# Optimization experiments

Hardware: AMD Instinct MI355X
Metric: run time of the kernel (lower is better)

Reference implementation:

```python
import jax, jax.numpy as jnp
import numpy as np

N_BINS = 64
INPUT_DIM = 8
R = 1.2
BOUND = 10.0
BETA = 1e-06
N = 2097152


def _mesh_and_elmt():
    m = N_BINS / 2
    idx = jnp.arange(N_BINS + 1, dtype=jnp.float32) - m
    x1L = BOUND * (R - 1.0) / (R ** m - 1.0)
    xr = (1.0 - R ** jnp.abs(idx)) / (1.0 - R)
    xr = jnp.where(idx >= 0, x1L * xr, -x1L * xr)
    xr = (xr + BOUND) / (2.0 * BOUND)
    mesh = jnp.concatenate([jnp.zeros((1,), jnp.float32), xr[1:-1], jnp.ones((1,), jnp.float32)])  # [n_bins+1]
    elmt = mesh[1:] - mesh[:-1]  # [n_bins]
    return mesh, elmt


def _pdf_normalize(p, elmt):
    # pdf: [n_bins+1, d]; F_ref: [n_bins, d] cumulative bin integrals
    p0 = jnp.full((1, INPUT_DIM), BETA, jnp.float32)
    ep = jnp.exp(p)
    px = ep * ((elmt[:-1] + elmt[1:]) / 2.0)[:, None]
    scale = (1.0 - (elmt[0] + elmt[-1]) * BETA / 2.0) / jnp.sum(px, 0, keepdims=True)
    px = scale * ep
    pdf = jnp.concatenate([p0, px, p0], 0)
    cell = (pdf[:-1] + pdf[1:]) / 2.0 * elmt[:, None]  # [n_bins, d]
    F_ref = jnp.concatenate([jnp.zeros((1, INPUT_DIM), jnp.float32),
                             jnp.cumsum(cell, 0)[:N_BINS - 1]], 0)
    return pdf, F_ref


def setup_inputs() -> dict:
    key = jax.random.key(0)
    k1, k2 = jax.random.split(key)
    x = jax.random.normal(k1, (N, INPUT_DIM), dtype=jnp.float32)
    logdet = jnp.zeros((N, 1), dtype=jnp.float32)
    p = jax.random.normal(k2, (N_BINS - 1, INPUT_DIM), dtype=jnp.float32)
    return {"x": x, "logdet": logdet, "p": p}


def reference(x, logdet, p):
    mesh, elmt = _mesh_and_elmt()
    pdf, F_ref = _pdf_normalize(p, elmt)

    xs = (x + BOUND) / (2.0 * BOUND)  # [N, d] in [0,1] for covered points
    k = jnp.searchsorted(mesh, xs, side='right') - 1  # [N, d]
    cover = (k >= 0) & (k <= N_BINS - 1)
    k = jnp.clip(k, 0, N_BINS - 1)
    col = jnp.arange(INPUT_DIM)[None, :]

    v1 = pdf[k, col]            # [N, d]
    v2 = pdf[k + 1, col]
    xm = xs - mesh[k]
    h = elmt[k]
    F_pre = F_ref[k, col]

    y = jnp.where(cover, F_pre + xm * xm / 2.0 * (v2 - v1) / h + xm * v1, xs)
    dld = jnp.where(cover, xm * (v2 - v1) / h + v1, 1.0)
    logdet = logdet + jnp.sum(jnp.log(dld), -1, keepdims=True)

    y = y * 2.0 * BOUND - BOUND
    y = jnp.where(y > BOUND, BETA * (y - BOUND) + BOUND, y)
    logdet = logdet + jnp.sum(jnp.log(jnp.where(y > BOUND, BETA, 1.0)), -1, keepdims=True)
    y = jnp.where(y < -BOUND, BETA * (y + BOUND) - BOUND, y)
    logdet = logdet + jnp.sum(jnp.log(jnp.where(y < -BOUND, BETA, 1.0)), -1, keepdims=True)
    return y, logdet
```

## Files before the change

### kernel.cpp

```cpp
#include <hip/hip_runtime.h>
#include <hip/hip_bf16.h>
#include <math.h>

#define NDIM   8
#define NBINS  64
#define LOG_BETA   (-13.815510557964274f)
#define LN2F       0.69314718055994531f
#define ALPHA      34.0821892f
#define INV_LOG2R  3.80178401692393f

__global__ __launch_bounds__(256, 8) void cdfq_fused(const float* __restrict__ x,
                                                     const float* __restrict__ logdet_in,
                                                     const float* __restrict__ p,
                                                     float* __restrict__ y_out,
                                                     float* __restrict__ ld_out,
                                                     int n)
{
    __shared__ float  mesh[65];
    __shared__ float  elmt[64];
    __shared__ float  sc[NDIM];
    __shared__ float  pdfs[NDIM][65];
    __shared__ float4 stbl[NDIM * NBINS];

    const int t  = threadIdx.x;
    const int T  = gridDim.x * blockDim.x;
    const int i0 = blockIdx.x * blockDim.x + t;
    const int iters = n / T;
    const float4* xv = (const float4*)x;

    float4 Ac, Bc; float Lc;
    if (iters > 0) {
        Ac = xv[2 * (size_t)i0];
        Bc = xv[2 * (size_t)i0 + 1];
        Lc = logdet_in[i0];
    }
    __builtin_amdgcn_sched_barrier(0);

    if (t < 65) {
        float fidx = (float)t - 32.0f;
        float a = fabsf(fidx);
        float x1L = 2.0f / (powf(1.2f, 32.0f) - 1.0f);
        float xr = x1L * (powf(1.2f, a) - 1.0f) / 0.2f;
        xr = (fidx >= 0.0f) ? xr : -xr;
        xr = (xr + 10.0f) / 20.0f;
        if (t == 0)  xr = 0.0f;
        if (t == 64) xr = 1.0f;
        mesh[t] = xr;
    }
    for (int idx = t; idx < 63 * NDIM; idx += 256) {
        int d = idx & 7, k = idx >> 3;
        pdfs[d][k + 1] = expf(p[k * NDIM + d]);
    }
    if (t < NDIM) { pdfs[t][0] = 1e-6f; pdfs[t][64] = 1e-6f; }
    __syncthreads();
    if (t < 64) elmt[t] = mesh[t + 1] - mesh[t];
    __syncthreads();

    if (t < 64) {
        for (int d = 0; d < NDIM; ++d) {
            float w = 0.0f;
            if (t < 63) w = pdfs[d][t + 1] * 0.5f * (elmt[t] + elmt[t + 1]);
            for (int off = 32; off > 0; off >>= 1) w += __shfl_down(w, off);
            if (t == 0) sc[d] = (1.0f - (elmt[0] + elmt[63]) * 5e-7f) / w;
        }
    }
    __syncthreads();
    for (int idx = t; idx < 63 * NDIM; idx += 256) {
        int d = idx & 7, k = idx >> 3;
        pdfs[d][k + 1] *= sc[d];
    }
    __syncthreads();
    if (t < 64) {
        for (int d = 0; d < NDIM; ++d) {
            float c0 = 0.5f * (pdfs[d][t] + pdfs[d][t + 1]) * elmt[t];
            float v = c0;
            for (int off = 1; off < 64; off <<= 1) {
                float w = __shfl_up(v, off);
                if (t >= off) v += w;
            }
            float Fpre = v - c0;
            float v1 = pdfs[d][t];
            float v2 = pdfs[d][t + 1];
            stbl[d * 64 + t] = make_float4(v1, (v2 - v1) / elmt[t], Fpre, mesh[t]);
        }
    }
    __syncthreads();

    auto body = [&](float4 A, float4 B, float Lin, int i) {
        float ld = Lin;
        float xd[8] = {A.x, A.y, A.z, A.w, B.x, B.y, B.z, B.w};
        float yd[8], dd[8];

#pragma unroll
        for (int d = 0; d < 8; ++d) {
            float xo = xd[d];
            float xs = fmaf(xo, 0.05f, 0.5f);
            float u  = fabsf(xo);
            float g  = __log2f(fmaf(ALPHA, u, 1.0f)) * INV_LOG2R;
            int jp = (int)fminf(g, 31.0f);
            int jn = (int)ceilf(fminf(g, 32.0f));
            int k  = (xo >= 0.0f) ? (32 + jp) : (32 - jn);

            float4 tb = stbl[(d << 6) + k];
            float xm  = xs - tb.w;
            bool cov  = (xs >= 0.0f) && (xs < 1.0f);

            float yc = tb.z + xm * fmaf(0.5f * xm, tb.y, tb.x);
            float dl = fmaf(xm, tb.y, tb.x);
            float yy = cov ? yc : xs;
            dd[d]    = cov ? dl : 1.0f;

            yy = fmaf(yy, 20.0f, -10.0f);
            if (yy > 10.0f)  { yy = fmaf(1e-6f, yy - 10.0f, 10.0f);  ld += LOG_BETA; }
            if (yy < -10.0f) { yy = fmaf(1e-6f, yy + 10.0f, -10.0f); ld += LOG_BETA; }
            yd[d] = yy;
        }

        float l01 = __log2f(dd[0] * dd[1]);
        float l23 = __log2f(dd[2] * dd[3]);
        float l45 = __log2f(dd[4] * dd[5]);
        float l67 = __log2f(dd[6] * dd[7]);
        ld = fmaf((l01 + l23) + (l45 + l67), LN2F, ld);

        float4* yo = (float4*)y_out + 2 * (size_t)i;
        yo[0] = make_float4(yd[0], yd[1], yd[2], yd[3]);
        yo[1] = make_float4(yd[4], yd[5], yd[6], yd[7]);
        ld_out[i] = ld;
    };

    for (int j = 0; j < iters; ++j) {
        float4 An, Bn; float Ln;
        const bool more = (j + 1 < iters);
        if (more) {
            size_t ix = (size_t)i0 + (size_t)(j + 1) * T;
            An = xv[2 * ix];
            Bn = xv[2 * ix + 1];
            Ln = logdet_in[ix];
        }
        __builtin_amdgcn_sched_barrier(0);

        body(Ac, Bc, Lc, i0 + j * T);

        if (more) { Ac = An; Bc = Bn; Lc = Ln; }
    }

    int ir = i0 + iters * T;
    if (ir < n) {
        float4 A = xv[2 * (size_t)ir];
        float4 B = xv[2 * (size_t)ir + 1];
        float  L = logdet_in[ir];
        body(A, B, L, ir);
    }
}

extern "C" void kernel_launch(void* const* d_in, const int* in_sizes, int n_in,
                              void* d_out, int out_size, void* d_ws, size_t ws_size,
                              hipStream_t stream) {
    const float* x      = (const float*)d_in[0];
    const float* logdet = (const float*)d_in[1];
    const float* p      = (const float*)d_in[2];

    const int n = in_sizes[1];
    float* y_out  = (float*)d_out;
    float* ld_out = (float*)d_out + (size_t)n * NDIM;

    const int block = 256;
    int grid = 2048;
    if (grid * block > n) grid = (n + block - 1) / block;
    cdfq_fused<<<grid, block, 0, stream>>>(x, logdet, p, y_out, ld_out, n);
}
```

Baseline: 139.6 us.

## Split each row across two threads with one float4 per thread

Each thread now handles half a row, four dimensions loaded as a single float4, instead of a full 8-dim row. The two halves' logdet contributions are combined with a lane shuffle, and the even thread writes the logdet. The intent is fully contiguous wavefront-wide 16-byte accesses and more parallel work per iteration, with shorter per-thread dependency chains. In exchange the logdet load is duplicated across thread pairs, a shuffle is added, and half the lanes sit idle on the logdet store.

```diff
diff --git a/kernel.cpp b/kernel.cpp
--- a/kernel.cpp
+++ b/kernel.cpp
@@ -25,14 +25,14 @@
     const int t  = threadIdx.x;
     const int T  = gridDim.x * blockDim.x;
     const int i0 = blockIdx.x * blockDim.x + t;
-    const int iters = n / T;
-    const float4* xv = (const float4*)x;
+    const int G  = 2 * n;
+    const int iters = G / T;
+    const float4* xv4 = (const float4*)x;
 
-    float4 Ac, Bc; float Lc;
+    float4 Xc; float Lc;
     if (iters > 0) {
-        Ac = xv[2 * (size_t)i0];
-        Bc = xv[2 * (size_t)i0 + 1];
-        Lc = logdet_in[i0];
+        Xc = xv4[i0];
+        Lc = logdet_in[i0 >> 1];
     }
     __builtin_amdgcn_sched_barrier(0);
 
@@ -86,70 +86,64 @@
     }
     __syncthreads();
 
-    auto body = [&](float4 A, float4 B, float Lin, int i) {
-        float ld = Lin;
-        float xd[8] = {A.x, A.y, A.z, A.w, B.x, B.y, B.z, B.w};
-        float yd[8], dd[8];
+    auto body = [&](float4 X, float Lin, int g) {
+        const int q     = g >> 1;
+        const int dbase = (g & 1) << 2;
+        float xd[4] = {X.x, X.y, X.z, X.w};
+        float yd[4], dd[4];
+        float extra = 0.0f;
 
 #pragma unroll
-        for (int d = 0; d < 8; ++d) {
-            float xo = xd[d];
+        for (int dl = 0; dl < 4; ++dl) {
+            float xo = xd[dl];
             float xs = fmaf(xo, 0.05f, 0.5f);
             float u  = fabsf(xo);
-            float g  = __log2f(fmaf(ALPHA, u, 1.0f)) * INV_LOG2R;
-            int jp = (int)fminf(g, 31.0f);
-            int jn = (int)ceilf(fminf(g, 32.0f));
+            float gg = __log2f(fmaf(ALPHA, u, 1.0f)) * INV_LOG2R;
+            int jp = (int)fminf(gg, 31.0f);
+            int jn = (int)ceilf(fminf(gg, 32.0f));
             int k  = (xo >= 0.0f) ? (32 + jp) : (32 - jn);
 
-            float4 tb = stbl[(d << 6) + k];
+            float4 tb = stbl[((dbase + dl) << 6) + k];
             float xm  = xs - tb.w;
             bool cov  = (xs >= 0.0f) && (xs < 1.0f);
 
             float yc = tb.z + xm * fmaf(0.5f * xm, tb.y, tb.x);
-            float dl = fmaf(xm, tb.y, tb.x);
+            float dv = fmaf(xm, tb.y, tb.x);
             float yy = cov ? yc : xs;
-            dd[d]    = cov ? dl : 1.0f;
+            dd[dl]   = cov ? dv : 1.0f;
 
             yy = fmaf(yy, 20.0f, -10.0f);
-            if (yy > 10.0f)  { yy = fmaf(1e-6f, yy - 10.0f, 10.0f);  ld += LOG_BETA; }
-            if (yy < -10.0f) { yy = fmaf(1e-6f, yy + 10.0f, -10.0f); ld += LOG_BETA; }
-            yd[d] = yy;
+            if (yy > 10.0f)  { yy = fmaf(1e-6f, yy - 10.0f, 10.0f);  extra += LOG_BETA; }
+            if (yy < -10.0f) { yy = fmaf(1e-6f, yy + 10.0f, -10.0f); extra += LOG_BETA; }
+            yd[dl] = yy;
         }
 
-        float l01 = __log2f(dd[0] * dd[1]);
-        float l23 = __log2f(dd[2] * dd[3]);
-        float l45 = __log2f(dd[4] * dd[5]);
-        float l67 = __log2f(dd[6] * dd[7]);
-        ld = fmaf((l01 + l23) + (l45 + l67), LN2F, ld);
+        float l2 = __log2f(dd[0] * dd[1]) + __log2f(dd[2] * dd[3]);
+        float contrib = fmaf(l2, LN2F, extra);
+        float cross   = __shfl_xor(contrib, 1);
 
-        float4* yo = (float4*)y_out + 2 * (size_t)i;
-        yo[0] = make_float4(yd[0], yd[1], yd[2], yd[3]);
-        yo[1] = make_float4(yd[4], yd[5], yd[6], yd[7]);
-        ld_out[i] = ld;
+        ((float4*)y_out)[g] = make_float4(yd[0], yd[1], yd[2], yd[3]);
+        if ((g & 1) == 0) ld_out[q] = Lin + contrib + cross;
     };
 
     for (int j = 0; j < iters; ++j) {
-        float4 An, Bn; float Ln;
+        float4 Xn; float Ln;
         const bool more = (j + 1 < iters);
         if (more) {
-            size_t ix = (size_t)i0 + (size_t)(j + 1) * T;
-            An = xv[2 * ix];
-            Bn = xv[2 * ix + 1];
-            Ln = logdet_in[ix];
+            int gx = i0 + (j + 1) * T;
+            Xn = xv4[gx];
+            Ln = logdet_in[gx >> 1];
         }
         __builtin_amdgcn_sched_barrier(0);
 
-        body(Ac, Bc, Lc, i0 + j * T);
+        body(Xc, Lc, i0 + j * T);
 
-        if (more) { Ac = An; Bc = Bn; Lc = Ln; }
+        if (more) { Xc = Xn; Lc = Ln; }
     }
 
-    int ir = i0 + iters * T;
-    if (ir < n) {
-        float4 A = xv[2 * (size_t)ir];
-        float4 B = xv[2 * (size_t)ir + 1];
-        float  L = logdet_in[ir];
-        body(A, B, L, ir);
+    int gr = i0 + iters * T;
+    if (gr < G) {
+        body(xv4[gr], logdet_in[gr >> 1], gr);
     }
 }
 
@@ -166,6 +160,6 @@
 
     const int block = 256;
     int grid = 2048;
-    if (grid * block > n) grid = (n + block - 1) / block;
+    if ((long long)grid * block > 2LL * n) grid = (2 * n + block - 1) / block;
     cdfq_fused<<<grid, block, 0, stream>>>(x, logdet, p, y_out, ld_out, n);
 }
```

Result: no change. 138.9 us (-0.5%).
